# Kernel tuning notes

Hardware: AMD Instinct MI355X
Metric: run time of the kernel (lower is better)

The kernel has to match this reference:

```python
import jax, jax.numpy as jnp
import numpy as np

N, K = 10000, 32          # nodes, max neighbors
NUM_ELEM = 100
D_ATOM = 128              # atom embedding size
D_DIR_IN, D_DIR = 10, 64  # node direction expansion -> embedding
D_DIST_IN, D_DIST = 128, 128  # edge distance expansion -> embedding


def setup_inputs() -> dict:
    key = jax.random.key(0)
    ks = jax.random.split(key, 12)
    inp = {
        "atomic_numbers": jax.random.randint(ks[0], (N,), 0, NUM_ELEM),
        "node_direction_expansion": jax.random.normal(ks[1], (N, D_DIR_IN), jnp.float32),
        "edge_distance_expansion": jax.random.normal(ks[2], (N, K, D_DIST_IN), jnp.float32),
        "neighbor_list": jax.random.randint(ks[3], (N, K), 0, N),
        "neighbor_mask": jax.random.randint(ks[4], (N, K), 0, 2).astype(bool),
        # learned params
        "src_atom_emb": jax.random.uniform(ks[5], (NUM_ELEM, D_ATOM), jnp.float32, -0.001, 0.001),
        "tgt_atom_emb": jax.random.uniform(ks[6], (NUM_ELEM, D_ATOM), jnp.float32, -0.001, 0.001),
        "src_dir_W": jax.random.normal(ks[7], (D_DIR_IN, D_DIR), jnp.float32) * 0.1,
        "src_dir_b": jnp.zeros((D_DIR,), jnp.float32),
        "tgt_dir_W": jax.random.normal(ks[8], (D_DIR_IN, D_DIR), jnp.float32) * 0.1,
        "tgt_dir_b": jnp.zeros((D_DIR,), jnp.float32),
        "dist_W": jax.random.normal(ks[9], (D_DIST_IN, D_DIST), jnp.float32) * 0.1,
        "dist_b": jnp.zeros((D_DIST,), jnp.float32),
    }
    return inp


def reference(atomic_numbers, node_direction_expansion, edge_distance_expansion,
              neighbor_list, neighbor_mask,
              src_atom_emb, tgt_atom_emb,
              src_dir_W, src_dir_b, tgt_dir_W, tgt_dir_b, dist_W, dist_b):
    # per-node embeddings
    sa = src_atom_emb[atomic_numbers]                      # [N, D_ATOM]
    ta = tgt_atom_emb[atomic_numbers]                      # [N, D_ATOM]
    sd = jax.nn.silu(node_direction_expansion @ src_dir_W + src_dir_b)  # [N, D_DIR]
    td = jax.nn.silu(node_direction_expansion @ tgt_dir_W + tgt_dir_b)  # [N, D_DIR]

    # map_sender_receiver_feature: sender gathered via neighbor_list, receiver broadcast
    sender_atom = sa[neighbor_list]                        # [N, K, D_ATOM]
    recv_atom = jnp.broadcast_to(ta[:, None, :], (N, K, D_ATOM))
    sender_dir = sd[neighbor_list]                         # [N, K, D_DIR]
    recv_dir = jnp.broadcast_to(td[:, None, :], (N, K, D_DIR))

    edist = jax.nn.silu(edge_distance_expansion @ dist_W + dist_b)  # [N, K, D_DIST]

    edge_features = jnp.concatenate(
        [edist, sender_dir, sender_atom, recv_dir, recv_atom], axis=-1)  # [N, K, 512]

    # masked mean over neighbors
    m = neighbor_mask.astype(edge_features.dtype)          # [N, K]
    count = m.sum(axis=1, keepdims=True) + 1e-5            # [N, 1]
    out = (edge_features * m[:, :, None]).sum(axis=1) / count  # [N, 512]
    return out
```

## Files before the change

### kernel.cpp

```cpp
#include <hip/hip_runtime.h>
#include <hip/hip_bf16.h>

#define NN 10000
#define KK 32
#define DDIRIN 10
#define DDIR 64
#define DD 128

typedef short bf16x8 __attribute__((ext_vector_type(8)));
typedef float f32x4  __attribute__((ext_vector_type(4)));
typedef float f32x2  __attribute__((ext_vector_type(2)));

__device__ __forceinline__ float silu_f(float x) { return x / (1.0f + __expf(-x)); }

__device__ __forceinline__ ushort2 pk_bf16(float a, float b) {
    __hip_bfloat162 h = __float22bfloat162_rn(float2{a, b});
    union { __hip_bfloat162 h; ushort2 u; } v; v.h = h;
    return v.u;
}

__global__ __launch_bounds__(256, 4) void fused_kernel(
    const int*   __restrict__ an,
    const float* __restrict__ nde,
    const float* __restrict__ edist,
    const int*   __restrict__ nl,
    const int*   __restrict__ nmask,
    const float* __restrict__ semb,
    const float* __restrict__ temb,
    const float* __restrict__ sW, const float* __restrict__ sb,
    const float* __restrict__ tW, const float* __restrict__ tb,
    const float* __restrict__ dW,
    const float* __restrict__ db,
    float* __restrict__ out)
{
    const int tid  = threadIdx.x;
    const int wid  = tid >> 6;
    const int lane = tid & 63;
    const int l15  = lane & 15;
    const int quad = lane >> 4;
    const int n0   = blockIdx.x * 2;

    const int snd  = wid >> 1;
    const int sub  = wid & 1;
    const int n    = n0 + snd;

    __shared__ __align__(16) short s_E[64 * 128];
    __shared__ float s_cnt[2];

    int j = 0, aj = 0; bool act = false;
    if (lane < KK) {
        j   = nl[n * KK + lane];
        act = (nmask[n * KK + lane] != 0);
    }
    unsigned long long bits = __ballot(act);
    int cnt = (int)__popcll(bits);
    if (sub == 0 && act) aj = an[j];
    if (sub == 0 && lane == 0) s_cnt[snd] = (float)cnt;

    bf16x8 bfrag[2][4];
    float  bias[2];
#pragma unroll
    for (int c2 = 0; c2 < 2; ++c2) {
        int ncol = (2 * wid + c2) * 16 + l15;
        bias[c2] = db[ncol];
#pragma unroll
        for (int t = 0; t < 4; ++t) {
            bf16x8 v;
#pragma unroll
            for (int j2 = 0; j2 < 4; ++j2) {
                int k0 = t * 32 + quad * 8 + 2 * j2;
                ushort2 u = pk_bf16(dW[k0 * DD + ncol], dW[(k0 + 1) * DD + ncol]);
                v[2 * j2]     = (short)u.x;
                v[2 * j2 + 1] = (short)u.y;
            }
            bfrag[c2][t] = v;
        }
    }

    {
        const f32x4* E4 = reinterpret_cast<const f32x4*>(edist + (size_t)n0 * (KK * DD));
        const int* nm = nmask + n0 * KK;
#pragma unroll
        for (int i = 0; i < 4; ++i) {
            int f0  = 2 * tid + 512 * i;
            int row = f0 >> 5;
            f32x4 a = __builtin_nontemporal_load(&E4[f0]);
            f32x4 b = __builtin_nontemporal_load(&E4[f0 + 1]);
            ushort2 u0 = pk_bf16(a[0], a[1]), u1 = pk_bf16(a[2], a[3]);
            ushort2 u2 = pk_bf16(b[0], b[1]), u3 = pk_bf16(b[2], b[3]);
            bf16x8 v;
            v[0] = (short)u0.x; v[1] = (short)u0.y; v[2] = (short)u1.x; v[3] = (short)u1.y;
            v[4] = (short)u2.x; v[5] = (short)u2.y; v[6] = (short)u3.x; v[7] = (short)u3.y;
            bf16x8 z;
#pragma unroll
            for (int q = 0; q < 8; ++q) z[q] = 0;
            v = (nm[row] != 0) ? v : z;
            int kb = tid & 15;
            int sw = kb ^ (row & 7);
            *reinterpret_cast<bf16x8*>(&s_E[row * 128 + sw * 8]) = v;
        }
    }
    __syncthreads();

    f32x4 acc[4][2];
#pragma unroll
    for (int rt = 0; rt < 4; ++rt)
#pragma unroll
        for (int c2 = 0; c2 < 2; ++c2)
#pragma unroll
            for (int g = 0; g < 4; ++g) acc[rt][c2][g] = 0.0f;

#pragma unroll
    for (int rt = 0; rt < 4; ++rt) {
        bf16x8 af[4];
        int r = rt * 16 + l15;
#pragma unroll
        for (int t = 0; t < 4; ++t) {
            int kb = (4 * t + quad) ^ (l15 & 7);
            af[t] = *reinterpret_cast<const bf16x8*>(&s_E[r * 128 + kb * 8]);
        }
#pragma unroll
        for (int t = 0; t < 4; ++t) {
            acc[rt][0] = __builtin_amdgcn_mfma_f32_16x16x32_bf16(af[t], bfrag[0][t], acc[rt][0], 0, 0, 0);
            acc[rt][1] = __builtin_amdgcn_mfma_f32_16x16x32_bf16(af[t], bfrag[1][t], acc[rt][1], 0, 0, 0);
        }
    }

#pragma unroll
    for (int c2 = 0; c2 < 2; ++c2) {
        float sbv = silu_f(bias[c2]);
#pragma unroll
        for (int nd = 0; nd < 2; ++nd) {
            float p = 0.0f;
#pragma unroll
            for (int h = 0; h < 2; ++h) {
                int rt = 2 * nd + h;
#pragma unroll
                for (int g = 0; g < 4; ++g)
                    p += silu_f(acc[rt][c2][g] + bias[c2]);
            }
            p += __shfl_xor(p, 16);
            p += __shfl_xor(p, 32);
            if (quad == nd) {
                float c = s_cnt[nd];
                float val = (p - (32.0f - c) * sbv) / (c + 1e-5f);
                __builtin_nontemporal_store(
                    val, &out[(size_t)(n0 + nd) * 512 + (2 * wid + c2) * 16 + l15]);
            }
        }
    }

    {
        const float invv  = 1.0f / ((float)cnt + 1e-5f);
        const float scale = (float)cnt * invv;
        float* outn = out + (size_t)n * 512;

        if (sub == 0) {
            float sw_r[DDIRIN];
#pragma unroll
            for (int q = 0; q < DDIRIN; ++q) sw_r[q] = sW[q * DDIR + lane];
            const float sbv = sb[lane];

            float sdir = 0.0f, sa0 = 0.0f, sa1 = 0.0f;
            unsigned long long rem = bits;
#pragma unroll 4
            for (int i = 0; i < cnt; ++i) {
                int src = __builtin_ctzll(rem); rem &= rem - 1ull;
                int jj = __shfl(j, src);
                int ja = __shfl(aj, src);
                const f32x2* x2 = reinterpret_cast<const f32x2*>(nde + (size_t)jj * DDIRIN);
                float a = sbv;
#pragma unroll
                for (int q = 0; q < 5; ++q) {
                    f32x2 xv = x2[q];
                    a = fmaf(xv[0], sw_r[2 * q], a);
                    a = fmaf(xv[1], sw_r[2 * q + 1], a);
                }
                sdir += silu_f(a);
                f32x2 e = reinterpret_cast<const f32x2*>(semb + (size_t)ja * DD)[lane];
                sa0 += e[0]; sa1 += e[1];
            }
            __builtin_nontemporal_store(sdir * invv, &outn[128 + lane]);
            f32x2 sa = {sa0 * invv, sa1 * invv};
            __builtin_nontemporal_store(sa, reinterpret_cast<f32x2*>(&outn[192 + 2 * lane]));
        } else {
            {
                const f32x2* x2 = reinterpret_cast<const f32x2*>(nde + (size_t)n * DDIRIN);
                float a = tb[lane];
#pragma unroll
                for (int q = 0; q < 5; ++q) {
                    f32x2 xv = x2[q];
                    a = fmaf(xv[0], tW[(2 * q) * DDIR + lane], a);
                    a = fmaf(xv[1], tW[(2 * q + 1) * DDIR + lane], a);
                }
                __builtin_nontemporal_store(silu_f(a) * scale, &outn[320 + lane]);
            }
            {
                int ann = an[n];
                f32x2 r = reinterpret_cast<const f32x2*>(temb + (size_t)ann * DD)[lane];
                f32x2 rv = {r[0] * scale, r[1] * scale};
                __builtin_nontemporal_store(rv, reinterpret_cast<f32x2*>(&outn[384 + 2 * lane]));
            }
        }
    }
}

extern "C" void kernel_launch(void* const* d_in, const int* in_sizes, int n_in,
                              void* d_out, int out_size, void* d_ws, size_t ws_size,
                              hipStream_t stream) {
    const int*   an    = (const int*)  d_in[0];
    const float* nde   = (const float*)d_in[1];
    const float* edist = (const float*)d_in[2];
    const int*   nl    = (const int*)  d_in[3];
    const int*   nmask = (const int*)  d_in[4];
    const float* semb  = (const float*)d_in[5];
    const float* temb  = (const float*)d_in[6];
    const float* sW    = (const float*)d_in[7];
    const float* sb    = (const float*)d_in[8];
    const float* tW    = (const float*)d_in[9];
    const float* tb    = (const float*)d_in[10];
    const float* dW    = (const float*)d_in[11];
    const float* db    = (const float*)d_in[12];
    float* out = (float*)d_out;

    fused_kernel<<<NN / 2, 256, 0, stream>>>(
        an, nde, edist, nl, nmask, semb, temb, sW, sb, tW, tb, dW, db, out);
}
```

Measured before the change: 292.9 us.

## Stream edge tile via async global-to-LDS loads and pre-convert weights to bf16

```diff
diff --git a/kernel.cpp b/kernel.cpp
--- a/kernel.cpp
+++ b/kernel.cpp
@@ -19,6 +19,25 @@
     return v.u;
 }
 
+__device__ __forceinline__ void gload_lds16(const void* g, void* l) {
+    typedef const unsigned int __attribute__((address_space(1)))* gp_t;
+    typedef unsigned int __attribute__((address_space(3)))* lp_t;
+    __builtin_amdgcn_global_load_lds(
+        (gp_t)(unsigned long long)g,
+        (lp_t)(unsigned int)(unsigned long long)l, 16, 0, 0);
+}
+
+__global__ __launch_bounds__(256) void prep_kernel(
+    const float* __restrict__ dW, ushort* __restrict__ dWb)
+{
+    int v = blockIdx.x * 256 + threadIdx.x;
+    int ncol = v >> 6;
+    int k0   = (v & 63) * 2;
+    ushort2 u = pk_bf16(dW[k0 * DD + ncol], dW[(k0 + 1) * DD + ncol]);
+    *reinterpret_cast<ushort2*>(&dWb[ncol * DD + k0]) = u;
+}
+
+template<bool PREB>
 __global__ __launch_bounds__(256, 4) void fused_kernel(
     const int*   __restrict__ an,
     const float* __restrict__ nde,
@@ -31,6 +50,7 @@
     const float* __restrict__ tW, const float* __restrict__ tb,
     const float* __restrict__ dW,
     const float* __restrict__ db,
+    const ushort* __restrict__ dWb,
     float* __restrict__ out)
 {
     const int tid  = threadIdx.x;
@@ -44,8 +64,20 @@
     const int sub  = wid & 1;
     const int n    = n0 + snd;
 
+    __shared__ __align__(16) float s_F[64 * 128];
     __shared__ __align__(16) short s_E[64 * 128];
     __shared__ float s_cnt[2];
+
+    {
+        const char* gbase = (const char*)(edist + (size_t)n0 * (KK * DD));
+#pragma unroll
+        for (int i = 0; i < 8; ++i) {
+            int s   = tid + 256 * i;
+            int gs  = s ^ ((s >> 5) & 7);
+            int sb0 = wid * 64 + 256 * i;
+            gload_lds16(gbase + (size_t)gs * 16, (char*)s_F + (size_t)sb0 * 16);
+        }
+    }
 
     int j = 0, aj = 0; bool act = false;
     if (lane < KK) {
@@ -59,33 +91,49 @@
 
     bf16x8 bfrag[2][4];
     float  bias[2];
-#pragma unroll
-    for (int c2 = 0; c2 < 2; ++c2) {
-        int ncol = (2 * wid + c2) * 16 + l15;
-        bias[c2] = db[ncol];
-#pragma unroll
-        for (int t = 0; t < 4; ++t) {
-            bf16x8 v;
-#pragma unroll
-            for (int j2 = 0; j2 < 4; ++j2) {
-                int k0 = t * 32 + quad * 8 + 2 * j2;
-                ushort2 u = pk_bf16(dW[k0 * DD + ncol], dW[(k0 + 1) * DD + ncol]);
-                v[2 * j2]     = (short)u.x;
-                v[2 * j2 + 1] = (short)u.y;
-            }
-            bfrag[c2][t] = v;
-        }
-    }
+    if constexpr (PREB) {
+#pragma unroll
+        for (int c2 = 0; c2 < 2; ++c2) {
+            int ncol = (2 * wid + c2) * 16 + l15;
+            bias[c2] = db[ncol];
+#pragma unroll
+            for (int t = 0; t < 4; ++t)
+                bfrag[c2][t] = *reinterpret_cast<const bf16x8*>(
+                    &dWb[ncol * DD + t * 32 + quad * 8]);
+        }
+    } else {
+#pragma unroll
+        for (int c2 = 0; c2 < 2; ++c2) {
+            int ncol = (2 * wid + c2) * 16 + l15;
+            bias[c2] = db[ncol];
+#pragma unroll
+            for (int t = 0; t < 4; ++t) {
+                bf16x8 v;
+#pragma unroll
+                for (int j2 = 0; j2 < 4; ++j2) {
+                    int k0 = t * 32 + quad * 8 + 2 * j2;
+                    ushort2 u = pk_bf16(dW[k0 * DD + ncol], dW[(k0 + 1) * DD + ncol]);
+                    v[2 * j2]     = (short)u.x;
+                    v[2 * j2 + 1] = (short)u.y;
+                }
+                bfrag[c2][t] = v;
+            }
+        }
+    }
+
+    __syncthreads();
 
     {
-        const f32x4* E4 = reinterpret_cast<const f32x4*>(edist + (size_t)n0 * (KK * DD));
-        const int* nm = nmask + n0 * KK;
-#pragma unroll
-        for (int i = 0; i < 4; ++i) {
-            int f0  = 2 * tid + 512 * i;
-            int row = f0 >> 5;
-            f32x4 a = __builtin_nontemporal_load(&E4[f0]);
-            f32x4 b = __builtin_nontemporal_load(&E4[f0 + 1]);
+        int r  = tid >> 2;
+        int q  = tid & 3;
+        int rx = r & 7;
+        bool on = (nmask[n0 * KK + r] != 0);
+#pragma unroll
+        for (int u = 0; u < 4; ++u) {
+            int ca = (q * 8 + 2 * u)     ^ rx;
+            int cb = (q * 8 + 2 * u + 1) ^ rx;
+            f32x4 a = *reinterpret_cast<const f32x4*>(&s_F[(r * 32 + ca) * 4]);
+            f32x4 b = *reinterpret_cast<const f32x4*>(&s_F[(r * 32 + cb) * 4]);
             ushort2 u0 = pk_bf16(a[0], a[1]), u1 = pk_bf16(a[2], a[3]);
             ushort2 u2 = pk_bf16(b[0], b[1]), u3 = pk_bf16(b[2], b[3]);
             bf16x8 v;
@@ -93,11 +141,9 @@
             v[4] = (short)u2.x; v[5] = (short)u2.y; v[6] = (short)u3.x; v[7] = (short)u3.y;
             bf16x8 z;
 #pragma unroll
-            for (int q = 0; q < 8; ++q) z[q] = 0;
-            v = (nm[row] != 0) ? v : z;
-            int kb = tid & 15;
-            int sw = kb ^ (row & 7);
-            *reinterpret_cast<bf16x8*>(&s_E[row * 128 + sw * 8]) = v;
+            for (int t = 0; t < 8; ++t) z[t] = 0;
+            v = on ? v : z;
+            *reinterpret_cast<bf16x8*>(&s_E[r * 128 + ((4 * q + u) ^ rx) * 8]) = v;
         }
     }
     __syncthreads();
@@ -223,6 +269,13 @@
     const float* db    = (const float*)d_in[12];
     float* out = (float*)d_out;
 
-    fused_kernel<<<NN / 2, 256, 0, stream>>>(
-        an, nde, edist, nl, nmask, semb, temb, sW, sb, tW, tb, dW, db, out);
-}
+    if (ws_size >= (size_t)DD * DD * sizeof(ushort)) {
+        ushort* dWb = (ushort*)d_ws;
+        prep_kernel<<<32, 256, 0, stream>>>(dW, dWb);
+        fused_kernel<true><<<NN / 2, 256, 0, stream>>>(
+            an, nde, edist, nl, nmask, semb, temb, sW, sb, tW, tb, dW, db, dWb, out);
+    } else {
+        fused_kernel<false><<<NN / 2, 256, 0, stream>>>(
+            an, nde, edist, nl, nmask, semb, temb, sW, sb, tW, tb, dW, db, nullptr, out);
+    }
+}
```

Result: slower. 302.1 us (+3.1%).

## Split kernel into persistent GEMM blocks and separate gather-segment blocks

Applied to the files above, without the earlier changes.

```diff
diff --git a/kernel.cpp b/kernel.cpp
--- a/kernel.cpp
+++ b/kernel.cpp
@@ -7,6 +7,9 @@
 #define DDIR 64
 #define DD 128
 
+#define GEMM_BLOCKS 768
+#define SEG_BLOCKS  (NN / 4)
+
 typedef short bf16x8 __attribute__((ext_vector_type(8)));
 typedef float f32x4  __attribute__((ext_vector_type(4)));
 typedef float f32x2  __attribute__((ext_vector_type(2)));
@@ -19,7 +22,7 @@
     return v.u;
 }
 
-__global__ __launch_bounds__(256, 4) void fused_kernel(
+__global__ __launch_bounds__(256, 3) void mega_kernel(
     const int*   __restrict__ an,
     const float* __restrict__ nde,
     const float* __restrict__ edist,
@@ -36,126 +39,159 @@
     const int tid  = threadIdx.x;
     const int wid  = tid >> 6;
     const int lane = tid & 63;
-    const int l15  = lane & 15;
-    const int quad = lane >> 4;
-    const int n0   = blockIdx.x * 2;
-
-    const int snd  = wid >> 1;
-    const int sub  = wid & 1;
-    const int n    = n0 + snd;
 
     __shared__ __align__(16) short s_E[64 * 128];
-    __shared__ float s_cnt[2];
-
-    int j = 0, aj = 0; bool act = false;
-    if (lane < KK) {
-        j   = nl[n * KK + lane];
-        act = (nmask[n * KK + lane] != 0);
+
+    if (blockIdx.x < GEMM_BLOCKS) {
+        const int l15  = lane & 15;
+        const int quad = lane >> 4;
+
+        const int NT     = NN / 2;
+        const int stride = GEMM_BLOCKS;
+        int tile = blockIdx.x;
+
+        f32x4 va[4], vb[4];
+        int   mval;
+        {
+            const f32x4* E4 = reinterpret_cast<const f32x4*>(edist) + (size_t)tile * 2048;
+#pragma unroll
+            for (int i = 0; i < 4; ++i) {
+                int f0 = 2 * tid + 512 * i;
+                va[i] = E4[f0];
+                vb[i] = E4[f0 + 1];
+            }
+            mval = nmask[tile * 64 + lane];
+        }
+
+        bf16x8 bfrag[2][4];
+        float  bias[2];
+#pragma unroll
+        for (int c2 = 0; c2 < 2; ++c2) {
+            int ncol = (2 * wid + c2) * 16 + l15;
+            bias[c2] = db[ncol];
+#pragma unroll
+            for (int t = 0; t < 4; ++t) {
+                bf16x8 v;
+#pragma unroll
+                for (int j2 = 0; j2 < 4; ++j2) {
+                    int k0 = t * 32 + quad * 8 + 2 * j2;
+                    ushort2 u = pk_bf16(dW[k0 * DD + ncol], dW[(k0 + 1) * DD + ncol]);
+                    v[2 * j2]     = (short)u.x;
+                    v[2 * j2 + 1] = (short)u.y;
+                }
+                bfrag[c2][t] = v;
+            }
+        }
+
+        while (true) {
+            const unsigned long long bits = __ballot(mval != 0);
+            const float cnt0 = (float)__popcll(bits & 0xffffffffull);
+            const float cnt1 = (float)__popcll(bits >> 32);
+            const int   n0   = tile * 2;
+
+#pragma unroll
+            for (int i = 0; i < 4; ++i) {
+                int row = (tid >> 4) + 16 * i;
+                f32x4 a = va[i], b = vb[i];
+                ushort2 u0 = pk_bf16(a[0], a[1]), u1 = pk_bf16(a[2], a[3]);
+                ushort2 u2 = pk_bf16(b[0], b[1]), u3 = pk_bf16(b[2], b[3]);
+                bf16x8 v;
+                v[0] = (short)u0.x; v[1] = (short)u0.y; v[2] = (short)u1.x; v[3] = (short)u1.y;
+                v[4] = (short)u2.x; v[5] = (short)u2.y; v[6] = (short)u3.x; v[7] = (short)u3.y;
+                bf16x8 z;
+#pragma unroll
+                for (int q = 0; q < 8; ++q) z[q] = 0;
+                v = ((bits >> row) & 1ull) ? v : z;
+                int kb = tid & 15;
+                int sw = kb ^ (row & 7);
+                *reinterpret_cast<bf16x8*>(&s_E[row * 128 + sw * 8]) = v;
+            }
+            __syncthreads();
+
+            const int  ntile = tile + stride;
+            const bool more  = (ntile < NT);
+            if (more) {
+                const f32x4* E4n = reinterpret_cast<const f32x4*>(edist) + (size_t)ntile * 2048;
+#pragma unroll
+                for (int i = 0; i < 4; ++i) {
+                    int f0 = 2 * tid + 512 * i;
+                    va[i] = E4n[f0];
+                    vb[i] = E4n[f0 + 1];
+                }
+                mval = nmask[ntile * 64 + lane];
+            }
+
+            f32x4 acc[4][2];
+#pragma unroll
+            for (int rt = 0; rt < 4; ++rt)
+#pragma unroll
+                for (int c2 = 0; c2 < 2; ++c2)
+#pragma unroll
+                    for (int g = 0; g < 4; ++g) acc[rt][c2][g] = 0.0f;
+
+#pragma unroll
+            for (int rt = 0; rt < 4; ++rt) {
+                bf16x8 af[4];
+                int r = rt * 16 + l15;
+#pragma unroll
+                for (int t = 0; t < 4; ++t) {
+                    int kb = (4 * t + quad) ^ (l15 & 7);
+                    af[t] = *reinterpret_cast<const bf16x8*>(&s_E[r * 128 + kb * 8]);
+                }
+#pragma unroll
+                for (int t = 0; t < 4; ++t) {
+                    acc[rt][0] = __builtin_amdgcn_mfma_f32_16x16x32_bf16(af[t], bfrag[0][t], acc[rt][0], 0, 0, 0);
+                    acc[rt][1] = __builtin_amdgcn_mfma_f32_16x16x32_bf16(af[t], bfrag[1][t], acc[rt][1], 0, 0, 0);
+                }
+            }
+
+#pragma unroll
+            for (int c2 = 0; c2 < 2; ++c2) {
+                float sbv = silu_f(bias[c2]);
+#pragma unroll
+                for (int nd = 0; nd < 2; ++nd) {
+                    float p = 0.0f;
+#pragma unroll
+                    for (int h = 0; h < 2; ++h) {
+                        int rt = 2 * nd + h;
+#pragma unroll
+                        for (int g = 0; g < 4; ++g)
+                            p += silu_f(acc[rt][c2][g] + bias[c2]);
+                    }
+                    p += __shfl_xor(p, 16);
+                    p += __shfl_xor(p, 32);
+                    if (quad == nd) {
+                        float c = (nd == 0) ? cnt0 : cnt1;
+                        float val = (p - (32.0f - c) * sbv) / (c + 1e-5f);
+                        out[(size_t)(n0 + nd) * 512 + (2 * wid + c2) * 16 + l15] = val;
+                    }
+                }
+            }
+
+            if (!more) break;
+            __syncthreads();
+            tile = ntile;
+        }
+        return;
     }
-    unsigned long long bits = __ballot(act);
-    int cnt = (int)__popcll(bits);
-    if (sub == 0 && act) aj = an[j];
-    if (sub == 0 && lane == 0) s_cnt[snd] = (float)cnt;
-
-    bf16x8 bfrag[2][4];
-    float  bias[2];
-#pragma unroll
-    for (int c2 = 0; c2 < 2; ++c2) {
-        int ncol = (2 * wid + c2) * 16 + l15;
-        bias[c2] = db[ncol];
-#pragma unroll
-        for (int t = 0; t < 4; ++t) {
-            bf16x8 v;
-#pragma unroll
-            for (int j2 = 0; j2 < 4; ++j2) {
-                int k0 = t * 32 + quad * 8 + 2 * j2;
-                ushort2 u = pk_bf16(dW[k0 * DD + ncol], dW[(k0 + 1) * DD + ncol]);
-                v[2 * j2]     = (short)u.x;
-                v[2 * j2 + 1] = (short)u.y;
-            }
-            bfrag[c2][t] = v;
-        }
-    }
 
     {
-        const f32x4* E4 = reinterpret_cast<const f32x4*>(edist + (size_t)n0 * (KK * DD));
-        const int* nm = nmask + n0 * KK;
-#pragma unroll
-        for (int i = 0; i < 4; ++i) {
-            int f0  = 2 * tid + 512 * i;
-            int row = f0 >> 5;
-            f32x4 a = __builtin_nontemporal_load(&E4[f0]);
-            f32x4 b = __builtin_nontemporal_load(&E4[f0 + 1]);
-            ushort2 u0 = pk_bf16(a[0], a[1]), u1 = pk_bf16(a[2], a[3]);
-            ushort2 u2 = pk_bf16(b[0], b[1]), u3 = pk_bf16(b[2], b[3]);
-            bf16x8 v;
-            v[0] = (short)u0.x; v[1] = (short)u0.y; v[2] = (short)u1.x; v[3] = (short)u1.y;
-            v[4] = (short)u2.x; v[5] = (short)u2.y; v[6] = (short)u3.x; v[7] = (short)u3.y;
-            bf16x8 z;
-#pragma unroll
-            for (int q = 0; q < 8; ++q) z[q] = 0;
-            v = (nm[row] != 0) ? v : z;
-            int kb = tid & 15;
-            int sw = kb ^ (row & 7);
-            *reinterpret_cast<bf16x8*>(&s_E[row * 128 + sw * 8]) = v;
-        }
-    }
-    __syncthreads();
-
-    f32x4 acc[4][2];
-#pragma unroll
-    for (int rt = 0; rt < 4; ++rt)
-#pragma unroll
-        for (int c2 = 0; c2 < 2; ++c2)
-#pragma unroll
-            for (int g = 0; g < 4; ++g) acc[rt][c2][g] = 0.0f;
-
-#pragma unroll
-    for (int rt = 0; rt < 4; ++rt) {
-        bf16x8 af[4];
-        int r = rt * 16 + l15;
-#pragma unroll
-        for (int t = 0; t < 4; ++t) {
-            int kb = (4 * t + quad) ^ (l15 & 7);
-            af[t] = *reinterpret_cast<const bf16x8*>(&s_E[r * 128 + kb * 8]);
-        }
-#pragma unroll
-        for (int t = 0; t < 4; ++t) {
-            acc[rt][0] = __builtin_amdgcn_mfma_f32_16x16x32_bf16(af[t], bfrag[0][t], acc[rt][0], 0, 0, 0);
-            acc[rt][1] = __builtin_amdgcn_mfma_f32_16x16x32_bf16(af[t], bfrag[1][t], acc[rt][1], 0, 0, 0);
-        }
-    }
-
-#pragma unroll
-    for (int c2 = 0; c2 < 2; ++c2) {
-        float sbv = silu_f(bias[c2]);
-#pragma unroll
-        for (int nd = 0; nd < 2; ++nd) {
-            float p = 0.0f;
-#pragma unroll
-            for (int h = 0; h < 2; ++h) {
-                int rt = 2 * nd + h;
-#pragma unroll
-                for (int g = 0; g < 4; ++g)
-                    p += silu_f(acc[rt][c2][g] + bias[c2]);
-            }
-            p += __shfl_xor(p, 16);
-            p += __shfl_xor(p, 32);
-            if (quad == nd) {
-                float c = s_cnt[nd];
-                float val = (p - (32.0f - c) * sbv) / (c + 1e-5f);
-                __builtin_nontemporal_store(
-                    val, &out[(size_t)(n0 + nd) * 512 + (2 * wid + c2) * 16 + l15]);
-            }
-        }
-    }
-
-    {
+        const int n = (blockIdx.x - GEMM_BLOCKS) * 4 + wid;
+
+        int j = 0, aj = 0; bool act = false;
+        if (lane < KK) {
+            j   = nl[n * KK + lane];
+            act = (nmask[n * KK + lane] != 0);
+        }
+        unsigned long long bits = __ballot(act);
+        int cnt = (int)__popcll(bits);
+        if (act) aj = an[j];
+
         const float invv  = 1.0f / ((float)cnt + 1e-5f);
         const float scale = (float)cnt * invv;
         float* outn = out + (size_t)n * 512;
 
-        if (sub == 0) {
+        {
             float sw_r[DDIRIN];
 #pragma unroll
             for (int q = 0; q < DDIRIN; ++q) sw_r[q] = sW[q * DDIR + lane];
@@ -180,27 +216,28 @@
                 f32x2 e = reinterpret_cast<const f32x2*>(semb + (size_t)ja * DD)[lane];
                 sa0 += e[0]; sa1 += e[1];
             }
-            __builtin_nontemporal_store(sdir * invv, &outn[128 + lane]);
+            outn[128 + lane] = sdir * invv;
             f32x2 sa = {sa0 * invv, sa1 * invv};
-            __builtin_nontemporal_store(sa, reinterpret_cast<f32x2*>(&outn[192 + 2 * lane]));
-        } else {
-            {
-                const f32x2* x2 = reinterpret_cast<const f32x2*>(nde + (size_t)n * DDIRIN);
-                float a = tb[lane];
-#pragma unroll
-                for (int q = 0; q < 5; ++q) {
-                    f32x2 xv = x2[q];
-                    a = fmaf(xv[0], tW[(2 * q) * DDIR + lane], a);
-                    a = fmaf(xv[1], tW[(2 * q + 1) * DDIR + lane], a);
-                }
-                __builtin_nontemporal_store(silu_f(a) * scale, &outn[320 + lane]);
-            }
-            {
-                int ann = an[n];
-                f32x2 r = reinterpret_cast<const f32x2*>(temb + (size_t)ann * DD)[lane];
-                f32x2 rv = {r[0] * scale, r[1] * scale};
-                __builtin_nontemporal_store(rv, reinterpret_cast<f32x2*>(&outn[384 + 2 * lane]));
-            }
+            *reinterpret_cast<f32x2*>(&outn[192 + 2 * lane]) = sa;
+        }
+
+        {
+            const f32x2* x2 = reinterpret_cast<const f32x2*>(nde + (size_t)n * DDIRIN);
+            float a = tb[lane];
+#pragma unroll
+            for (int q = 0; q < 5; ++q) {
+                f32x2 xv = x2[q];
+                a = fmaf(xv[0], tW[(2 * q) * DDIR + lane], a);
+                a = fmaf(xv[1], tW[(2 * q + 1) * DDIR + lane], a);
+            }
+            outn[320 + lane] = silu_f(a) * scale;
+        }
+
+        {
+            int ann = an[n];
+            f32x2 r = reinterpret_cast<const f32x2*>(temb + (size_t)ann * DD)[lane];
+            f32x2 rv = {r[0] * scale, r[1] * scale};
+            *reinterpret_cast<f32x2*>(&outn[384 + 2 * lane]) = rv;
         }
     }
 }
@@ -223,6 +260,6 @@
     const float* db    = (const float*)d_in[12];
     float* out = (float*)d_out;
 
-    fused_kernel<<<NN / 2, 256, 0, stream>>>(
+    mega_kernel<<<GEMM_BLOCKS + SEG_BLOCKS, 256, 0, stream>>>(
         an, nde, edist, nl, nmask, semb, temb, sW, sb, tW, tb, dW, db, out);
 }
```

Measured after the change: 289.4 us. Within noise of the previous version (-1.2%).
